# Optimization experiments

Measured on AMD Instinct MI355X. Metric: run time of the kernel, lower is better.

The kernel has to match this reference:

```python
import jax, jax.numpy as jnp
import numpy as np

M = 41  # window length (odd)


def _triplet_index(M):
    half = M // 2
    S = [(m, n, k)
         for m in range(-half, half + 1)
         for n in range(-half, half + 1)
         for k in range(-half, half + 1)
         if abs(m) <= half and abs(n) <= half and abs(k) <= half and abs(m + n) <= half]
    return np.asarray(S, dtype=np.int32)  # [T, 3]


def setup_inputs() -> dict:
    key = jax.random.key(0)
    k1, k2 = jax.random.split(key)
    B = 128
    E_real = jax.random.normal(k1, (B, M, 2), dtype=jnp.float32)
    E_imag = jax.random.normal(k2, (B, M, 2), dtype=jnp.float32)
    return {"E_real": E_real, "E_imag": E_imag}


def reference(E_real, E_imag):
    E = E_real + 1j * E_imag  # [B, M, Nmodes] complex
    idx = _triplet_index(M)
    m, n, k = idx[:, 0], idx[:, 1], idx[:, 2]
    B, Mlen, Nmodes = E.shape
    p = Mlen // 2
    # triplets(E, m, n) = E[p+m] * E[p+n] * conj(E[p+m+n])  -> [B, T, Nmodes]
    Em = E[:, p + m, :]
    En = E[:, p + n, :]
    Emn = E[:, p + m + n, :]
    E1 = Em * En * jnp.conj(Emn)
    Ek = E[:, p + k, :]   # [B, T, Nmodes]
    Enk = E[:, p - k, :]
    # term1 = sum_modes |E[p+k]|^2 ; term2 = sum_modes E[p+k]*E[p-k]
    term1 = jnp.sum(Ek.real ** 2 + Ek.imag ** 2, axis=-1)  # [B, T] real
    term2 = jnp.sum(Ek * Enk, axis=-1)                      # [B, T] complex
    feat1 = E1 * term1[..., None]             # [B, T, Nmodes]
    feat2 = jnp.conj(E1) * term2[..., None]   # [B, T, Nmodes]
    # torch stacks [feat1_t, feat2_t, feat1_{t+1}, ...] along last dim -> [B, Nmodes, 2T]
    pair = jnp.stack([feat1, feat2], axis=-1)           # [B, T, Nmodes, 2]
    out = jnp.transpose(pair, (0, 2, 1, 3)).reshape(B, Nmodes, -1)
    return out
```

## Files before the change

### kernel.cpp

```cpp
#include <hip/hip_runtime.h>
#include <hip/hip_bf16.h>

#define M41    41
#define HALF   20
#define NPAIR  1261
#define NTRIP  (NPAIR * M41)
#define NGRP   12925
#define P_PER_B (NGRP + 1)
#define QSLOTS 28

#if defined(__has_builtin)
# if __has_builtin(__builtin_amdgcn_cvt_pk_bf16_f32)
#  define HAVE_PK_BF16 1
# endif
#endif

static __device__ __forceinline__ unsigned short f2bf_sw(float f) {
    unsigned int u = __float_as_uint(f);
    unsigned int r = u + 0x7fffu + ((u >> 16) & 1u);
    return (unsigned short)(r >> 16);
}
static __device__ __forceinline__ unsigned int pk2(float lo, float hi) {
#ifdef HAVE_PK_BF16
    typedef __bf16 bf2 __attribute__((ext_vector_type(2)));
    union { bf2 v; unsigned int u; } cv;
    cv.v = __builtin_amdgcn_cvt_pk_bf16_f32(lo, hi);
    return cv.u;
#else
    return (unsigned int)f2bf_sw(lo) | ((unsigned int)f2bf_sw(hi) << 16);
#endif
}

static __device__ __forceinline__ int pair_decode(int q) {
    int qq = q; bool flip = false;
    if (qq >= 651) { qq = 1260 - qq; flip = true; }
    float x = sqrtf(1681.0f + 8.0f * (float)qq);
    int mi = (int)((x - 41.0f) * 0.5f);
    if (mi < 0) mi = 0;
    while (((mi + 1) * (mi + 42)) / 2 <= qq) ++mi;
    while ((mi * (mi + 41)) / 2 > qq)       --mi;
    int off = qq - (mi * (mi + 41)) / 2;
    int ni  = off + (HALF - mi);
    if (flip) { mi = 40 - mi; ni = 40 - ni; }
    return mi | (ni << 8) | ((mi + ni - HALF) << 16);
}

static __device__ __forceinline__ float2 e1_of(const float2 (*sE)[2], int d, int c) {
    float2 a  = sE[d & 255][c];
    float2 bb = sE[(d >> 8) & 255][c];
    float2 dd = sE[(d >> 16) & 255][c];
    float2 ab = make_float2(a.x*bb.x - a.y*bb.y, a.x*bb.y + a.y*bb.x);
    return make_float2(ab.x*dd.x + ab.y*dd.y, ab.y*dd.x - ab.x*dd.y);
}

static __device__ __forceinline__ uint2 feat(float2 E1, float t1, float2 t2) {
    uint2 r;
    r.x = pk2(E1.x * t1, E1.y * t1);
    r.y = pk2(E1.x*t2.x + E1.y*t2.y, E1.x*t2.y - E1.y*t2.x);
    return r;
}

__global__ __launch_bounds__(256) void so_features(
    const float* __restrict__ E_real, const float* __restrict__ E_imag,
    unsigned int* __restrict__ out)
{
    __shared__ float2 sE[M41][2];
    __shared__ float  sT1[M41];
    __shared__ float2 sT2[M41];
    __shared__ float2 sE1[QSLOTS][2];

    const int b   = blockIdx.y;
    const int tid = threadIdx.x;
    const int q_lo = (1024 * blockIdx.x) / M41;

    if (tid < 2 * M41) {
        int base = b * (2 * M41) + tid;
        sE[tid >> 1][tid & 1] = make_float2(E_real[base], E_imag[base]);
    }
    __syncthreads();

    if (tid < M41) {
        float2 e0 = sE[tid][0], e1 = sE[tid][1];
        sT1[tid] = e0.x*e0.x + e0.y*e0.y + e1.x*e1.x + e1.y*e1.y;
        float2 g0 = sE[40 - tid][0], g1 = sE[40 - tid][1];
        sT2[tid] = make_float2(
            e0.x*g0.x - e0.y*g0.y + e1.x*g1.x - e1.y*g1.y,
            e0.x*g0.y + e0.y*g0.x + e1.x*g1.y + e1.y*g1.x);
    } else if (tid >= 64 && tid < 64 + QSLOTS) {
        int q = q_lo + (tid - 64);
        if (q <= NPAIR - 1) {
            int d = pair_decode(q);
            sE1[tid - 64][0] = e1_of(sE, d, 0);
            sE1[tid - 64][1] = e1_of(sE, d, 1);
        }
    }
    __syncthreads();

    int p = blockIdx.x * 256 + tid;
    if (p >= P_PER_B) return;

    const size_t base0 = (size_t)(b * 2 + 0) * (2 * NTRIP);
    const size_t base1 = (size_t)(b * 2 + 1) * (2 * NTRIP);

    if (p == NGRP) {
        int dA = pair_decode(NPAIR - 1);
        uint2 vA = feat(e1_of(sE, dA, 0), sT1[40], sT2[40]);
        *(uint2*)&out[base0 + 2 * (size_t)(NTRIP - 1)] = vA;
        int dB = pair_decode(0);
        uint2 vB = feat(e1_of(sE, dB, 1), sT1[0], sT2[0]);
        *(uint2*)&out[base1] = vB;
        return;
    }

    int t0 = 4 * p;
    int q0 = t0 / M41;
    int k  = t0 - q0 * M41;
    int dq = q0 - q_lo;

    unsigned int A[8], Bv[8];
    #pragma unroll
    for (int j = 0; j < 5; ++j) {
        float  t1v = sT1[k];
        float2 t2v = sT2[k];
        if (j < 4) {
            uint2 f = feat(sE1[dq][0], t1v, t2v);
            A[2*j] = f.x; A[2*j + 1] = f.y;
        }
        if (j > 0) {
            uint2 f = feat(sE1[dq][1], t1v, t2v);
            Bv[2*(j-1)] = f.x; Bv[2*j - 1] = f.y;
        }
        if (++k == M41) { k = 0; ++dq; }
    }

    uint4 v;
    size_t i0 = base0 + 2 * (size_t)t0;
    v.x = A[0]; v.y = A[1]; v.z = A[2]; v.w = A[3];
    *(uint4*)&out[i0] = v;
    v.x = A[4]; v.y = A[5]; v.z = A[6]; v.w = A[7];
    *(uint4*)&out[i0 + 4] = v;

    size_t i1 = base1 + 2 * (size_t)t0 + 2;
    v.x = Bv[0]; v.y = Bv[1]; v.z = Bv[2]; v.w = Bv[3];
    *(uint4*)&out[i1] = v;
    v.x = Bv[4]; v.y = Bv[5]; v.z = Bv[6]; v.w = Bv[7];
    *(uint4*)&out[i1 + 4] = v;
}

extern "C" void kernel_launch(void* const* d_in, const int* in_sizes, int n_in,
                              void* d_out, int out_size, void* d_ws, size_t ws_size,
                              hipStream_t stream) {
    const float* E_imag = (const float*)d_in[0];
    const float* E_real = (const float*)d_in[1];
    unsigned int* out = (unsigned int*)d_out;

    int B = in_sizes[0] / (2 * M41);

    dim3 grid((P_PER_B + 255) / 256, B);
    so_features<<<grid, 256, 0, stream>>>(E_real, E_imag, out);
}
```

Measured before the change: 118.5 us.

## Stage outputs in shared memory for coalesced stores in both mode planes

Each thread now computes both mode planes for the same four triplets, so the one-element offset on the second plane is no longer handled per thread. Results go to LDS staging buffers and are then written back as contiguous, coalesced 16-byte and 8-byte stores per block. The goal is to avoid the misaligned and strided global stores on the output plane. The cost is a second barrier, 16 KB of LDS per block, and separate handling of the tail triplet and the partial last block.

Result: faster. 114.0 us (-3.8%).

```diff
diff --git a/kernel.cpp b/kernel.cpp
--- a/kernel.cpp
+++ b/kernel.cpp
@@ -5,8 +5,6 @@
 #define HALF   20
 #define NPAIR  1261
 #define NTRIP  (NPAIR * M41)
-#define NGRP   12925
-#define P_PER_B (NGRP + 1)
 #define QSLOTS 28
 
 #if defined(__has_builtin)
@@ -68,10 +66,13 @@
     __shared__ float  sT1[M41];
     __shared__ float2 sT2[M41];
     __shared__ float2 sE1[QSLOTS][2];
+    __shared__ uint4  stA[512];
+    __shared__ uint4  stB[512];
 
-    const int b   = blockIdx.y;
-    const int tid = threadIdx.x;
-    const int q_lo = (1024 * blockIdx.x) / M41;
+    const int b     = blockIdx.y;
+    const int tid   = threadIdx.x;
+    const int tbase = blockIdx.x << 10;
+    const int q_lo  = tbase / M41;
 
     if (tid < 2 * M41) {
         int base = b * (2 * M41) + tid;
@@ -96,55 +97,56 @@
     }
     __syncthreads();
 
-    int p = blockIdx.x * 256 + tid;
-    if (p >= P_PER_B) return;
+    const int nvalid = min(1024, (NTRIP - 1) - tbase);
+    const int t0 = tbase + 4 * tid;
+    char* const oc = (char*)out;
+    const size_t plane = 8ull * (size_t)NTRIP;
+    const size_t pb0 = (size_t)(2*b)     * plane + 8ull * (size_t)tbase;
+    const size_t pb1 = (size_t)(2*b + 1) * plane + 8ull * (size_t)tbase;
 
-    const size_t base0 = (size_t)(b * 2 + 0) * (2 * NTRIP);
-    const size_t base1 = (size_t)(b * 2 + 1) * (2 * NTRIP);
+    if (4 * tid < nvalid) {
+        int q0 = t0 / M41;
+        int k  = t0 - q0 * M41;
+        int dq = q0 - q_lo;
+        unsigned int A[8], Bv[8];
+        #pragma unroll
+        for (int j = 0; j < 4; ++j) {
+            float  t1v = sT1[k];
+            float2 t2v = sT2[k];
+            uint2 fA = feat(sE1[dq][0], t1v, t2v);
+            uint2 fB = feat(sE1[dq][1], t1v, t2v);
+            A[2*j]  = fA.x;  A[2*j + 1]  = fA.y;
+            Bv[2*j] = fB.x;  Bv[2*j + 1] = fB.y;
+            if (++k == M41) { k = 0; ++dq; }
+        }
+        stA[2*tid]     = make_uint4(A[0],  A[1],  A[2],  A[3]);
+        stA[2*tid + 1] = make_uint4(A[4],  A[5],  A[6],  A[7]);
+        stB[2*tid]     = make_uint4(Bv[0], Bv[1], Bv[2], Bv[3]);
+        stB[2*tid + 1] = make_uint4(Bv[4], Bv[5], Bv[6], Bv[7]);
+    } else if (t0 == NTRIP - 1) {
+        int dq = (NPAIR - 1) - q_lo;
+        uint2 vA = feat(sE1[dq][0], sT1[40], sT2[40]);
+        uint2 vB = feat(sE1[dq][1], sT1[40], sT2[40]);
+        *(uint2*)(oc + (size_t)(2*b)     * plane + 8ull * (size_t)(NTRIP - 1)) = vA;
+        *(uint2*)(oc + (size_t)(2*b + 1) * plane + 8ull * (size_t)(NTRIP - 1)) = vB;
+    }
+    __syncthreads();
 
-    if (p == NGRP) {
-        int dA = pair_decode(NPAIR - 1);
-        uint2 vA = feat(e1_of(sE, dA, 0), sT1[40], sT2[40]);
-        *(uint2*)&out[base0 + 2 * (size_t)(NTRIP - 1)] = vA;
-        int dB = pair_decode(0);
-        uint2 vB = feat(e1_of(sE, dB, 1), sT1[0], sT2[0]);
-        *(uint2*)&out[base1] = vB;
-        return;
+    const uint2* sB2 = (const uint2*)stB;
+    if (nvalid == 1024) {
+        *(uint4*)(oc + pb0 +        16u * tid) = stA[tid];
+        *(uint4*)(oc + pb0 + 4096 + 16u * tid) = stA[tid + 256];
+        *(uint2*)(oc + pb1 +         8u * tid) = sB2[tid];
+        *(uint2*)(oc + pb1 + 2048 +  8u * tid) = sB2[tid + 256];
+        *(uint2*)(oc + pb1 + 4096 +  8u * tid) = sB2[tid + 512];
+        *(uint2*)(oc + pb1 + 6144 +  8u * tid) = sB2[tid + 768];
+    } else {
+        const int nu4 = nvalid >> 1;
+        for (int u = tid; u < nu4; u += 256)
+            *(uint4*)(oc + pb0 + 16u * (unsigned)u) = stA[u];
+        for (int u = tid; u < nvalid; u += 256)
+            *(uint2*)(oc + pb1 + 8u * (unsigned)u) = sB2[u];
     }
-
-    int t0 = 4 * p;
-    int q0 = t0 / M41;
-    int k  = t0 - q0 * M41;
-    int dq = q0 - q_lo;
-
-    unsigned int A[8], Bv[8];
-    #pragma unroll
-    for (int j = 0; j < 5; ++j) {
-        float  t1v = sT1[k];
-        float2 t2v = sT2[k];
-        if (j < 4) {
-            uint2 f = feat(sE1[dq][0], t1v, t2v);
-            A[2*j] = f.x; A[2*j + 1] = f.y;
-        }
-        if (j > 0) {
-            uint2 f = feat(sE1[dq][1], t1v, t2v);
-            Bv[2*(j-1)] = f.x; Bv[2*j - 1] = f.y;
-        }
-        if (++k == M41) { k = 0; ++dq; }
-    }
-
-    uint4 v;
-    size_t i0 = base0 + 2 * (size_t)t0;
-    v.x = A[0]; v.y = A[1]; v.z = A[2]; v.w = A[3];
-    *(uint4*)&out[i0] = v;
-    v.x = A[4]; v.y = A[5]; v.z = A[6]; v.w = A[7];
-    *(uint4*)&out[i0 + 4] = v;
-
-    size_t i1 = base1 + 2 * (size_t)t0 + 2;
-    v.x = Bv[0]; v.y = Bv[1]; v.z = Bv[2]; v.w = Bv[3];
-    *(uint4*)&out[i1] = v;
-    v.x = Bv[4]; v.y = Bv[5]; v.z = Bv[6]; v.w = Bv[7];
-    *(uint4*)&out[i1 + 4] = v;
 }
 
 extern "C" void kernel_launch(void* const* d_in, const int* in_sizes, int n_in,
@@ -156,6 +158,6 @@
 
     int B = in_sizes[0] / (2 * M41);
 
-    dim3 grid((P_PER_B + 255) / 256, B);
+    dim3 grid((NTRIP + 1023) / 1024, B);
     so_features<<<grid, 256, 0, stream>>>(E_real, E_imag, out);
 }
```
